# Performance work log

Measured on AMD Instinct MI355X. Metric: run time of the kernel, lower is better.

The kernel has to match this reference:

```python
import jax, jax.numpy as jnp
import numpy as np

B, S, E, H, D, P = 4, 2048, 1024, 16, 64, 64  # batch, seq, embed, heads, head_dim, position_dim
MASKED_BIAS = -10000.0


def setup_inputs() -> dict:
    key = jax.random.key(0)
    ks = jax.random.split(key, 24)
    n = lambda k, sh: jax.random.normal(k, sh, dtype=jnp.float32)
    eyeD = jnp.eye(D, dtype=jnp.float32)
    eyeH = jnp.eye(H, dtype=jnp.float32)
    inp = {
        'hidden_states': n(ks[0], (B, S, E)),
        'position_states': n(ks[1], (B, S, P)),
        # Conv2D per-head projections (identity init + perturbation): [H, D, D]
        'Wq': eyeD[None] + 0.02 * n(ks[2], (H, D, D)), 'bq': 0.01 * n(ks[3], (H, D)),
        'Wk': eyeD[None] + 0.02 * n(ks[4], (H, D, D)), 'bk': 0.01 * n(ks[5], (H, D)),
        'Wv': eyeD[None] + 0.02 * n(ks[6], (H, D, D)), 'bv': 0.01 * n(ks[7], (H, D)),
        # Conv2D(transpose=True) cross-head mix: weight [H_out, H_in, D], bias [H, D]
        'Wqh': eyeH[:, :, None] + 0.02 * n(ks[8], (H, H, D)), 'bqh': 0.01 * n(ks[9], (H, D)),
        'Wkh': eyeH[:, :, None] + 0.02 * n(ks[10], (H, H, D)), 'bkh': 0.01 * n(ks[11], (H, D)),
        'Wvh': eyeH[:, :, None] + 0.02 * n(ks[12], (H, H, D)), 'bvh': 0.01 * n(ks[13], (H, D)),
        # p_attn Conv1D: position_dim -> 3*head_dim
        'Wp': 0.02 * n(ks[14], (P, 3 * D)), 'bp': 0.01 * n(ks[15], (3 * D,)),
        # position_conv expand: weight [3, 1, H], bias [H]
        'Wpe': 0.02 * n(ks[16], (3, 1, H)), 'bpe': 0.01 * n(ks[17], (H,)),
        # c_proj Conv1D: E -> E
        'Wc': 0.02 * n(ks[18], (E, E)), 'bc': 0.01 * n(ks[19], (E,)),
    }
    return inp


def _attention(hidden_states, position_states, Wq, bq, Wqh, bqh, Wk, bk, Wkh, bkh,
               Wv, bv, Wvh, bvh, Wp, bp, Wpe, bpe, Wc, bc):
    b, s, _ = hidden_states.shape
    x = hidden_states.reshape(b, s, H, D)

    def proj(Wa, ba, Wh, bh):
        # Conv2D: per-head linear within head_dim
        y = jnp.einsum('bshd,hde->bshe', x, Wa) + ba
        # Conv2D(transpose): mix across heads, per feature dim d
        return jnp.einsum('bshd,ghd->bsgd', y, Wh) + bh

    q = proj(Wq, bq, Wqh, bqh)  # [b,s,H,D]
    k = proj(Wk, bk, Wkh, bkh)
    v = proj(Wv, bv, Wvh, bvh)

    # p_attn (Conv1D) -> [b,s,3,D]; p_expand broadcasts each var across heads
    p = (position_states @ Wp + bp).reshape(b, s, 3, D)
    pe = p[..., None, :] * Wpe[:, 0, :][:, :, None] + bpe[:, None]  # [b,s,3,H,D]
    q = q + pe[:, :, 0]
    k = k + pe[:, :, 1]
    v = v + pe[:, :, 2]

    q = q.transpose(0, 2, 1, 3)  # [b,H,s,D]
    k = k.transpose(0, 2, 1, 3)
    v = v.transpose(0, 2, 1, 3)

    scores = jnp.einsum('bhqd,bhkd->bhqk', q, k) / jnp.sqrt(jnp.float32(D))
    causal = jnp.tril(jnp.ones((s, s), dtype=bool))
    scores = jnp.where(causal, scores, jnp.float32(MASKED_BIAS))
    w = jax.nn.softmax(scores, axis=-1)
    o = jnp.einsum('bhqk,bhkd->bhqd', w, v)
    o = o.transpose(0, 2, 1, 3).reshape(b, s, E)
    return o @ Wc + bc


def reference(hidden_states, position_states, Wq, bq, Wqh, bqh, Wk, bk, Wkh, bkh,
              Wv, bv, Wvh, bvh, Wp, bp, Wpe, bpe, Wc, bc):
    return _attention(hidden_states, position_states, Wq, bq, Wqh, bqh, Wk, bk,
                      Wkh, bkh, Wv, bv, Wvh, bvh, Wp, bp, Wpe, bpe, Wc, bc)
```

## Files before the change

kernel.cpp:

```cpp
#include <hip/hip_runtime.h>
#include <stdint.h>
#include <stddef.h>

using bf16x8 = __attribute__((ext_vector_type(8))) __bf16;
using f32x4  = __attribute__((ext_vector_type(4))) float;
using u16x8  = __attribute__((ext_vector_type(8))) unsigned short;
using u16x4  = __attribute__((ext_vector_type(4))) unsigned short;
typedef unsigned short u16;

#define DEV __device__ __forceinline__

#define QSCALE 0.18033688011112042f
#define SBIAS 32.0f

DEV u16 f2bf(float f) {
  unsigned u = __float_as_uint(f);
  u += 0x7fffu + ((u >> 16) & 1u);
  return (u16)(u >> 16);
}

DEV void gld_lds16(const u16* g, u16* l) {
  __builtin_amdgcn_global_load_lds(
      (__attribute__((address_space(1))) void*)g,
      (__attribute__((address_space(3))) void*)l, 16, 0, 0);
}

__global__ __launch_bounds__(256) void k_prep(const float* __restrict__ hs, const float* __restrict__ ps,
                                              const float* __restrict__ Wq, const float* __restrict__ Wk,
                                              const float* __restrict__ Wv, const float* __restrict__ Wqh,
                                              const float* __restrict__ Wkh, const float* __restrict__ Wvh,
                                              const float* __restrict__ Wp, const float* __restrict__ Wpe,
                                              const float* __restrict__ bq, const float* __restrict__ bk,
                                              const float* __restrict__ bv, const float* __restrict__ bqh,
                                              const float* __restrict__ bkh, const float* __restrict__ bvh,
                                              const float* __restrict__ bp, const float* __restrict__ bpe,
                                              const float* __restrict__ Wc,
                                              u16* __restrict__ A, u16* __restrict__ Wt,
                                              float* __restrict__ bias, u16* __restrict__ WcT) {
  const int bid = blockIdx.x;
  if (bid < 8704) {
    int idx = bid * 256 + threadIdx.x;
    int t  = idx / 272;
    int c4 = (idx - t * 272) * 4;
    float4 f;
    if (c4 < 1024) f = *(const float4*)(hs + (size_t)t * 1024 + c4);
    else           f = *(const float4*)(ps + (size_t)t * 64 + (c4 - 1024));
    u16x4 o4;
    o4[0] = f2bf(f.x); o4[1] = f2bf(f.y); o4[2] = f2bf(f.z); o4[3] = f2bf(f.w);
    *(u16x4*)(A + (size_t)t * 1088 + c4) = o4;
  } else if (bid < 21760) {
    int idx = (bid - 8704) * 256 + threadIdx.x;
    int n = idx / 1088, kk = idx - n * 1088;
    int which = n >> 10, g = (n >> 6) & 15, e = n & 63;
    const float* Wa = (which == 0) ? Wq : (which == 1) ? Wk : Wv;
    const float* Wh = (which == 0) ? Wqh : (which == 1) ? Wkh : Wvh;
    float val;
    if (kk < 1024) {
      int h = kk >> 6, d = kk & 63;
      val = Wa[(size_t)(h * 64 + d) * 64 + e] * Wh[(size_t)(g * 16 + h) * 64 + e];
    } else {
      int p = kk - 1024;
      val = Wp[(size_t)p * 192 + which * 64 + e] * Wpe[which * 16 + g];
    }
    if (which == 0) val *= QSCALE;
    Wt[idx] = f2bf(val);
  } else if (bid < 21772) {
    int n = (bid - 21760) * 256 + threadIdx.x;
    int which = n >> 10, g = (n >> 6) & 15, e = n & 63;
    const float* ba = (which == 0) ? bq : (which == 1) ? bk : bv;
    const float* Wh = (which == 0) ? Wqh : (which == 1) ? Wkh : Wvh;
    const float* bh = (which == 0) ? bqh : (which == 1) ? bkh : bvh;
    float s = bh[g * 64 + e] + bp[which * 64 + e] * Wpe[which * 16 + g] + bpe[g];
    for (int h = 0; h < 16; ++h) s += ba[h * 64 + e] * Wh[(g * 16 + h) * 64 + e];
    if (which == 0) s *= QSCALE;
    bias[n] = s;
  } else {
    __shared__ float tile[32][33];
    int t = bid - 21772;
    int tx = threadIdx.x & 31, ty = threadIdx.x >> 5;
    int n0 = (t & 31) * 32, k0 = (t >> 5) * 32;
#pragma unroll
    for (int i = 0; i < 32; i += 8)
      tile[ty + i][tx] = Wc[(size_t)(k0 + ty + i) * 1024 + n0 + tx];
    __syncthreads();
#pragma unroll
    for (int i = 0; i < 32; i += 8)
      WcT[(size_t)(n0 + ty + i) * 1024 + k0 + tx] = f2bf(tile[tx][ty + i]);
  }
}

template <int EPI>
__global__ __launch_bounds__(256) void gemm128(const u16* __restrict__ A, const u16* __restrict__ Bt,
                                               const float* __restrict__ bias,
                                               u16* __restrict__ qo, u16* __restrict__ ko, u16* __restrict__ vo,
                                               float* __restrict__ outf, int M, int N, int K, int NT) {
  __shared__ alignas(16) u16 As[2][8192];
  __shared__ alignas(16) u16 Bs[2][8192];
  const int tid = threadIdx.x;
  const int l = tid & 63, w = tid >> 6;
  const int lr = l & 15, lg = l >> 4;
  const int wm = w >> 1, wn = w & 1;

  const int nwg = gridDim.x;
  const int cpx = nwg >> 3;
  const int virt = (blockIdx.x & 7) * cpx + (blockIdx.x >> 3);
  const int m0 = (virt / NT) * 128, n0 = (virt - (virt / NT) * NT) * 128;

  const int KT = K >> 6;

  f32x4 acc[4][4] = {};

#pragma unroll
  for (int call = 0; call < 4; ++call) {
    int ci = (call * 4 + w) * 64 + l;
    int row = ci >> 3, s = ci & 7;
    int kq = (s ^ (row & 7)) * 8;
    gld_lds16(A + (size_t)(m0 + row) * K + kq, &As[0][(call * 4 + w) * 512]);
    gld_lds16(Bt + (size_t)(n0 + row) * K + kq, &Bs[0][(call * 4 + w) * 512]);
  }

  int cur = 0;
  for (int kt = 0; kt < KT; ++kt) {
    if (kt + 1 < KT) {
      const int kb = (kt + 1) * 64;
#pragma unroll
      for (int call = 0; call < 4; ++call) {
        int ci = (call * 4 + w) * 64 + l;
        int row = ci >> 3, s = ci & 7;
        int kq = (s ^ (row & 7)) * 8;
        gld_lds16(A + (size_t)(m0 + row) * K + kb + kq, &As[cur ^ 1][(call * 4 + w) * 512]);
        gld_lds16(Bt + (size_t)(n0 + row) * K + kb + kq, &Bs[cur ^ 1][(call * 4 + w) * 512]);
      }
      asm volatile("s_waitcnt vmcnt(8)" ::: "memory");
    } else {
      asm volatile("s_waitcnt vmcnt(0)" ::: "memory");
    }
    __builtin_amdgcn_s_barrier();
    asm volatile("" ::: "memory");

    const u16* AsC = As[cur];
    const u16* BsC = Bs[cur];
#pragma unroll
    for (int kk = 0; kk < 2; ++kk) {
      bf16x8 af[4], bfr[4];
#pragma unroll
      for (int mf = 0; mf < 4; ++mf) {
        int row = wm * 64 + mf * 16 + lr;
        int byo = row * 128 + (((kk * 32 + lg * 8) * 2) ^ ((row & 7) << 4));
        af[mf] = *(const bf16x8*)((const char*)AsC + byo);
      }
#pragma unroll
      for (int nf = 0; nf < 4; ++nf) {
        int row = wn * 64 + nf * 16 + lr;
        int byo = row * 128 + (((kk * 32 + lg * 8) * 2) ^ ((row & 7) << 4));
        bfr[nf] = *(const bf16x8*)((const char*)BsC + byo);
      }
      __builtin_amdgcn_s_setprio(1);
#pragma unroll
      for (int mf = 0; mf < 4; ++mf)
#pragma unroll
        for (int nf = 0; nf < 4; ++nf)
          acc[mf][nf] = __builtin_amdgcn_mfma_f32_16x16x32_bf16(af[mf], bfr[nf], acc[mf][nf], 0, 0, 0);
      __builtin_amdgcn_s_setprio(0);
    }

    asm volatile("s_waitcnt lgkmcnt(0)" ::: "memory");
    __builtin_amdgcn_s_barrier();
    asm volatile("" ::: "memory");
    cur ^= 1;
  }

#pragma unroll
  for (int mf = 0; mf < 4; ++mf)
#pragma unroll
    for (int nf = 0; nf < 4; ++nf)
#pragma unroll
      for (int r = 0; r < 4; ++r) {
        int row = m0 + wm * 64 + mf * 16 + lg * 4 + r;
        int col = n0 + wn * 64 + nf * 16 + lr;
        float val = acc[mf][nf][r] + bias[col];
        if (EPI == 0) {
          int which = col >> 10, g = (col >> 6) & 15, e = col & 63;
          int b = row >> 11, si = row & 2047;
          size_t idx = ((size_t)((b * 16 + g) * 2048 + si)) * 64 + e;
          u16 bvv = f2bf(val);
          if (which == 0) qo[idx] = bvv;
          else if (which == 1) ko[idx] = bvv;
          else vo[idx] = bvv;
        } else {
          outf[(size_t)row * N + col] = val;
        }
      }
}

__global__ __launch_bounds__(256) void k_transV(const u16* __restrict__ v, u16* __restrict__ vT) {
  __shared__ u16 t[64][65];
  int bh = blockIdx.y, s0 = blockIdx.x * 64;
  const u16* src = v + ((size_t)bh * 2048 + s0) * 64;
  u16* dst = vT + (size_t)bh * 64 * 2048 + s0;
  int tid = threadIdx.x;
#pragma unroll
  for (int it = 0; it < 2; ++it) {
    int ci = it * 256 + tid;
    int row = ci >> 3, sl = ci & 7;
    u16x8 val = *(const u16x8*)(src + (size_t)row * 64 + sl * 8);
#pragma unroll
    for (int jj = 0; jj < 8; ++jj) t[row][sl * 8 + jj] = val[jj];
  }
  __syncthreads();
#pragma unroll
  for (int it = 0; it < 2; ++it) {
    int ci = it * 256 + tid;
    int d = ci >> 3, sl = ci & 7;
    u16x8 val;
#pragma unroll
    for (int jj = 0; jj < 8; ++jj) {
      int cp = sl * 8 + jj;
      int tt = (cp & 3) * 16 + (cp >> 2);
      val[jj] = t[tt][d];
    }
    *(u16x8*)(dst + (size_t)d * 2048 + sl * 8) = val;
  }
}

__global__ __launch_bounds__(512) void k_attn(const u16* __restrict__ q, const u16* __restrict__ k,
                                              const u16* __restrict__ vt, u16* __restrict__ o) {
  __shared__ alignas(16) u16 Ks[2][4096];
  __shared__ alignas(16) u16 Vs[2][4096];
  __shared__ alignas(16) u16 Ps[8][32 * 72];

  const int tid = threadIdx.x, l = tid & 63, w = tid >> 6;
  const int lr = l & 15, lg = l >> 4;
  const int i = blockIdx.x;
  const int bh = (i & 7) * 8 + ((i >> 3) & 7);
  const int tile = 7 - (i >> 6);
  const int b = bh >> 4, h = bh & 15;

  const u16* qp = q + (size_t)bh * 2048 * 64;
  const u16* kp = k + (size_t)bh * 2048 * 64;
  const u16* vp = vt + (size_t)bh * 64 * 2048;

  const int srow = tid >> 3;
  const int skq = ((tid & 7) ^ (srow & 7)) * 8;

  bf16x8 ones;
#pragma unroll
  for (int e = 0; e < 8; ++e) ones[e] = (__bf16)1.0f;

  const int qr0 = tile * 256 + w * 32;
  const int jmax = 4 * tile + 3;
  const int jmask = qr0 >> 6;

  bf16x8 qf[2][2];
#pragma unroll
  for (int mf = 0; mf < 2; ++mf)
#pragma unroll
    for (int kk = 0; kk < 2; ++kk)
      qf[mf][kk] = *(const bf16x8*)(qp + (size_t)(qr0 + mf * 16 + lr) * 64 + kk * 32 + lg * 8);

  f32x4 oacc[2][4] = {};
  f32x4 osum[2] = {};

  gld_lds16(kp + (size_t)srow * 64 + skq, &Ks[0][w * 512]);
  gld_lds16(vp + (size_t)srow * 2048 + skq, &Vs[0][w * 512]);

  int cur = 0;
  for (int j = 0; j <= jmax; ++j) {
    if (j < jmax) {
      const int jn = j + 1;
      gld_lds16(kp + (size_t)(jn * 64 + srow) * 64 + skq, &Ks[cur ^ 1][w * 512]);
      gld_lds16(vp + (size_t)srow * 2048 + jn * 64 + skq, &Vs[cur ^ 1][w * 512]);
      asm volatile("s_waitcnt vmcnt(2)" ::: "memory");
    } else {
      asm volatile("s_waitcnt vmcnt(0)" ::: "memory");
    }
    __builtin_amdgcn_s_barrier();
    asm volatile("" ::: "memory");

    if (j <= jmask) {
      const u16* KsC = Ks[cur];
      const u16* VsC = Vs[cur];

      f32x4 sfr[2][4];
#pragma unroll
      for (int mf = 0; mf < 2; ++mf)
#pragma unroll
        for (int nf = 0; nf < 4; ++nf)
          sfr[mf][nf] = f32x4{-SBIAS, -SBIAS, -SBIAS, -SBIAS};
#pragma unroll
      for (int kk = 0; kk < 2; ++kk) {
        bf16x8 bk[4];
#pragma unroll
        for (int nf = 0; nf < 4; ++nf) {
          int row = nf * 16 + lr;
          int byo = row * 128 + (((kk * 32 + lg * 8) * 2) ^ ((row & 7) << 4));
          bk[nf] = *(const bf16x8*)((const char*)KsC + byo);
        }
        __builtin_amdgcn_s_setprio(1);
#pragma unroll
        for (int mf = 0; mf < 2; ++mf)
#pragma unroll
          for (int nf = 0; nf < 4; ++nf)
            sfr[mf][nf] = __builtin_amdgcn_mfma_f32_16x16x32_bf16(qf[mf][kk], bk[nf], sfr[mf][nf], 0, 0, 0);
        __builtin_amdgcn_s_setprio(0);
      }

      const bool maskt = (j == jmask);
#pragma unroll
      for (int mf = 0; mf < 2; ++mf)
#pragma unroll
        for (int r = 0; r < 4; ++r) {
          float s0 = sfr[mf][0][r], s1 = sfr[mf][1][r], s2 = sfr[mf][2][r], s3 = sfr[mf][3][r];
          if (maskt) {
            int rowg = qr0 + mf * 16 + lg * 4 + r;
            int base = j * 64 + lr;
            if (base      > rowg) s0 = -1e30f;
            if (base + 16 > rowg) s1 = -1e30f;
            if (base + 32 > rowg) s2 = -1e30f;
            if (base + 48 > rowg) s3 = -1e30f;
          }
          float p0 = __builtin_amdgcn_exp2f(s0);
          float p1 = __builtin_amdgcn_exp2f(s1);
          float p2 = __builtin_amdgcn_exp2f(s2);
          float p3 = __builtin_amdgcn_exp2f(s3);
          unsigned w0, w1;
          asm("v_cvt_pk_bf16_f32 %0, %1, %2" : "=v"(w0) : "v"(p0), "v"(p1));
          asm("v_cvt_pk_bf16_f32 %0, %1, %2" : "=v"(w1) : "v"(p2), "v"(p3));
          uint2 pw; pw.x = w0; pw.y = w1;
          *(uint2*)&Ps[w][(mf * 16 + lg * 4 + r) * 72 + 4 * lr] = pw;
        }

#pragma unroll
      for (int kk = 0; kk < 2; ++kk) {
        bf16x8 pa[2];
#pragma unroll
        for (int mf = 0; mf < 2; ++mf)
          pa[mf] = *(const bf16x8*)&Ps[w][(mf * 16 + lr) * 72 + kk * 32 + lg * 8];
        bf16x8 bv[4];
#pragma unroll
        for (int df = 0; df < 4; ++df) {
          int row = df * 16 + lr;
          int byo = row * 128 + (((kk * 32 + lg * 8) * 2) ^ ((row & 7) << 4));
          bv[df] = *(const bf16x8*)((const char*)VsC + byo);
        }
        __builtin_amdgcn_s_setprio(1);
#pragma unroll
        for (int mf = 0; mf < 2; ++mf)
#pragma unroll
          for (int df = 0; df < 4; ++df)
            oacc[mf][df] = __builtin_amdgcn_mfma_f32_16x16x32_bf16(pa[mf], bv[df], oacc[mf][df], 0, 0, 0);
#pragma unroll
        for (int mf = 0; mf < 2; ++mf)
          osum[mf] = __builtin_amdgcn_mfma_f32_16x16x32_bf16(pa[mf], ones, osum[mf], 0, 0, 0);
        __builtin_amdgcn_s_setprio(0);
      }
    }

    asm volatile("s_waitcnt lgkmcnt(0)" ::: "memory");
    __builtin_amdgcn_s_barrier();
    asm volatile("" ::: "memory");
    cur ^= 1;
  }

#pragma unroll
  for (int mf = 0; mf < 2; ++mf)
#pragma unroll
    for (int r = 0; r < 4; ++r) {
      float inv = 1.0f / osum[mf][r];
      int rowg = qr0 + mf * 16 + lg * 4 + r;
#pragma unroll
      for (int df = 0; df < 4; ++df)
        o[((size_t)(b * 2048 + rowg)) * 1024 + h * 64 + df * 16 + lr] = f2bf(oacc[mf][df][r] * inv);
    }
}

extern "C" void kernel_launch(void* const* d_in, const int* in_sizes, int n_in,
                              void* d_out, int out_size, void* d_ws, size_t ws_size,
                              hipStream_t stream) {
  const float* hs  = (const float*)d_in[0];
  const float* pos = (const float*)d_in[1];
  const float* Wq  = (const float*)d_in[2];  const float* bq  = (const float*)d_in[3];
  const float* Wk  = (const float*)d_in[4];  const float* bk  = (const float*)d_in[5];
  const float* Wv  = (const float*)d_in[6];  const float* bv  = (const float*)d_in[7];
  const float* Wqh = (const float*)d_in[8];  const float* bqh = (const float*)d_in[9];
  const float* Wkh = (const float*)d_in[10]; const float* bkh = (const float*)d_in[11];
  const float* Wvh = (const float*)d_in[12]; const float* bvh = (const float*)d_in[13];
  const float* Wp  = (const float*)d_in[14]; const float* bp  = (const float*)d_in[15];
  const float* Wpe = (const float*)d_in[16]; const float* bpe = (const float*)d_in[17];
  const float* Wc  = (const float*)d_in[18]; const float* bc  = (const float*)d_in[19];
  float* out = (float*)d_out;
  char* ws = (char*)d_ws;

  u16*   Abf   = (u16*)  (ws + 0);
  u16*   WT    = (u16*)  (ws + 17825792);
  float* biasq = (float*)(ws + 24510464);
  u16*   WcT   = (u16*)  (ws + 24522752);
  u16*   qb_   = (u16*)  (ws + 26619904);
  u16*   kb_   = (u16*)  (ws + 43397120);
  u16*   vb_   = (u16*)  (ws + 60174336);
  u16*   vTb   = (u16*)  (ws + 76951552);
  u16*   ob    = Abf;

  k_prep<<<22796, 256, 0, stream>>>(hs, pos, Wq, Wk, Wv, Wqh, Wkh, Wvh, Wp, Wpe,
                                    bq, bk, bv, bqh, bkh, bvh, bp, bpe, Wc,
                                    Abf, WT, biasq, WcT);
  gemm128<0><<<1536, 256, 0, stream>>>(Abf, WT, biasq, qb_, kb_, vb_, nullptr, 8192, 3072, 1088, 24);
  k_transV<<<dim3(32, 64), 256, 0, stream>>>(vb_, vTb);
  k_attn<<<512, 512, 0, stream>>>(qb_, kb_, vTb, ob);
  gemm128<1><<<512, 256, 0, stream>>>(ob, WcT, bc, nullptr, nullptr, nullptr, out, 8192, 1024, 1024, 8);
}
```

Measured before the change: 185.2 us.

## Replace QKV GEMM with 256x192-tile 512-thread kernel and split-phase staging

Adds a dedicated QKV projection GEMM that uses 256x192 output tiles with 8 waves and 512 blocks, replacing the 128x128 tile, 1536-block launch. Staging of the next K tile is split into B and two A halves, interleaved with four compute phases under barriers and vmcnt waits. The larger tiles raise arithmetic intensity and reduce redundant global reads, and 512 blocks map to a single wave of workgroups across the CUs. In exchange it uses about 112KB of LDS and more accumulator registers, which lowers occupancy. The generic gemm128 is reduced to the output-projection epilogue only.

```diff
diff --git a/kernel.cpp b/kernel.cpp
--- a/kernel.cpp
+++ b/kernel.cpp
@@ -89,10 +89,122 @@
   }
 }
 
-template <int EPI>
+__global__ __launch_bounds__(512) void gemmQKV(const u16* __restrict__ A, const u16* __restrict__ Bt,
+                                               const float* __restrict__ bias,
+                                               u16* __restrict__ qo, u16* __restrict__ ko, u16* __restrict__ vo,
+                                               int K) {
+  __shared__ alignas(16) u16 As[2][16384];
+  __shared__ alignas(16) u16 Bs[2][12288];
+  const int tid = threadIdx.x;
+  const int l = tid & 63, w = tid >> 6;
+  const int lr = l & 15, lg = l >> 4;
+  const int wm = w >> 2, wn = w & 3;
+
+  const int virt = (blockIdx.x & 7) * 64 + (blockIdx.x >> 3);
+  const int m0 = (virt >> 4) * 256, n0 = (virt & 15) * 192;
+
+#define STAGE_B(buf, kt) do {                                                  \
+  _Pragma("unroll")                                                            \
+  for (int c = 0; c < 3; ++c) {                                                \
+    int ci = c * 512 + tid;                                                    \
+    int srow = ci >> 3, s = ci & 7;                                            \
+    int kq = (s ^ (srow & 7)) * 8;                                             \
+    gld_lds16(Bt + (size_t)(n0 + srow) * K + (kt) * 64 + kq,                   \
+              &Bs[buf][(c * 8 + w) * 512]);                                    \
+  } } while (0)
+
+#define STAGE_A(buf, h, kt) do {                                               \
+  _Pragma("unroll")                                                            \
+  for (int c = 0; c < 2; ++c) {                                                \
+    int ci = c * 512 + tid;                                                    \
+    int srow = ci >> 3, s = ci & 7;                                            \
+    int g = (h) * 64 + (srow & 63) + (srow >> 6) * 128;                        \
+    int kq = (s ^ (srow & 7)) * 8;                                             \
+    gld_lds16(A + (size_t)(m0 + g) * K + (kt) * 64 + kq,                       \
+              &As[buf][(h) * 8192 + (c * 8 + w) * 512]);                       \
+  } } while (0)
+
+  f32x4 acc[8][3] = {};
+
+#define PHASE(buf, mh, kk) do {                                                \
+  bf16x8 af[4], bfr[3];                                                        \
+  _Pragma("unroll")                                                            \
+  for (int mq = 0; mq < 4; ++mq) {                                             \
+    int lrow = (mh) * 128 + wm * 64 + mq * 16 + lr;                            \
+    int byo = lrow * 128 + ((((kk) * 32 + lg * 8) * 2) ^ ((lrow & 7) << 4));   \
+    af[mq] = *(const bf16x8*)((const char*)As[buf] + byo);                     \
+  }                                                                            \
+  _Pragma("unroll")                                                            \
+  for (int nf = 0; nf < 3; ++nf) {                                             \
+    int brow = wn * 48 + nf * 16 + lr;                                         \
+    int byo = brow * 128 + ((((kk) * 32 + lg * 8) * 2) ^ ((brow & 7) << 4));   \
+    bfr[nf] = *(const bf16x8*)((const char*)Bs[buf] + byo);                    \
+  }                                                                            \
+  __builtin_amdgcn_s_setprio(1);                                               \
+  _Pragma("unroll")                                                            \
+  for (int mq = 0; mq < 4; ++mq)                                               \
+    _Pragma("unroll")                                                          \
+    for (int nf = 0; nf < 3; ++nf)                                             \
+      acc[(mh) * 4 + mq][nf] = __builtin_amdgcn_mfma_f32_16x16x32_bf16(        \
+          af[mq], bfr[nf], acc[(mh) * 4 + mq][nf], 0, 0, 0);                   \
+  __builtin_amdgcn_s_setprio(0);                                               \
+} while (0)
+
+  STAGE_B(0, 0);
+  STAGE_A(0, 0, 0);
+  STAGE_A(0, 1, 0);
+
+  const int KT = 17;
+  for (int t = 0; t < KT; ++t) {
+    const int buf = t & 1;
+    asm volatile("s_waitcnt vmcnt(2)" ::: "memory");
+    __builtin_amdgcn_s_barrier();
+    asm volatile("" ::: "memory");
+    if (t + 1 < KT) STAGE_B(buf ^ 1, t + 1);
+    PHASE(buf, 0, 0);
+    __builtin_amdgcn_s_barrier();
+    asm volatile("" ::: "memory");
+    if (t + 1 < KT) STAGE_A(buf ^ 1, 0, t + 1);
+    PHASE(buf, 0, 1);
+    if (t + 1 < KT) {
+      asm volatile("s_waitcnt vmcnt(5)" ::: "memory");
+    } else {
+      asm volatile("s_waitcnt vmcnt(0)" ::: "memory");
+    }
+    __builtin_amdgcn_s_barrier();
+    asm volatile("" ::: "memory");
+    if (t + 1 < KT) STAGE_A(buf ^ 1, 1, t + 1);
+    PHASE(buf, 1, 0);
+    __builtin_amdgcn_s_barrier();
+    asm volatile("" ::: "memory");
+    PHASE(buf, 1, 1);
+  }
+
+#undef PHASE
+#undef STAGE_A
+#undef STAGE_B
+
+#pragma unroll
+  for (int mf = 0; mf < 8; ++mf)
+#pragma unroll
+    for (int nf = 0; nf < 3; ++nf)
+#pragma unroll
+      for (int r = 0; r < 4; ++r) {
+        int row = m0 + wm * 128 + (mf >> 2) * 64 + (mf & 3) * 16 + lg * 4 + r;
+        int col = n0 + wn * 48 + nf * 16 + lr;
+        float val = acc[mf][nf][r] + bias[col];
+        int which = col >> 10, g = (col >> 6) & 15, e = col & 63;
+        int b = row >> 11, si = row & 2047;
+        size_t idx = ((size_t)((b * 16 + g) * 2048 + si)) * 64 + e;
+        u16 bvv = f2bf(val);
+        if (which == 0) qo[idx] = bvv;
+        else if (which == 1) ko[idx] = bvv;
+        else vo[idx] = bvv;
+      }
+}
+
 __global__ __launch_bounds__(256) void gemm128(const u16* __restrict__ A, const u16* __restrict__ Bt,
                                                const float* __restrict__ bias,
-                                               u16* __restrict__ qo, u16* __restrict__ ko, u16* __restrict__ vo,
                                                float* __restrict__ outf, int M, int N, int K, int NT) {
   __shared__ alignas(16) u16 As[2][8192];
   __shared__ alignas(16) u16 Bs[2][8192];
@@ -178,18 +290,7 @@
       for (int r = 0; r < 4; ++r) {
         int row = m0 + wm * 64 + mf * 16 + lg * 4 + r;
         int col = n0 + wn * 64 + nf * 16 + lr;
-        float val = acc[mf][nf][r] + bias[col];
-        if (EPI == 0) {
-          int which = col >> 10, g = (col >> 6) & 15, e = col & 63;
-          int b = row >> 11, si = row & 2047;
-          size_t idx = ((size_t)((b * 16 + g) * 2048 + si)) * 64 + e;
-          u16 bvv = f2bf(val);
-          if (which == 0) qo[idx] = bvv;
-          else if (which == 1) ko[idx] = bvv;
-          else vo[idx] = bvv;
-        } else {
-          outf[(size_t)row * N + col] = val;
-        }
+        outf[(size_t)row * N + col] = acc[mf][nf][r] + bias[col];
       }
 }
 
@@ -404,8 +505,8 @@
   k_prep<<<22796, 256, 0, stream>>>(hs, pos, Wq, Wk, Wv, Wqh, Wkh, Wvh, Wp, Wpe,
                                     bq, bk, bv, bqh, bkh, bvh, bp, bpe, Wc,
                                     Abf, WT, biasq, WcT);
-  gemm128<0><<<1536, 256, 0, stream>>>(Abf, WT, biasq, qb_, kb_, vb_, nullptr, 8192, 3072, 1088, 24);
+  gemmQKV<<<512, 512, 0, stream>>>(Abf, WT, biasq, qb_, kb_, vb_, 1088);
   k_transV<<<dim3(32, 64), 256, 0, stream>>>(vb_, vTb);
   k_attn<<<512, 512, 0, stream>>>(qb_, kb_, vTb, ob);
-  gemm128<1><<<512, 256, 0, stream>>>(ob, WcT, bc, nullptr, nullptr, nullptr, out, 8192, 1024, 1024, 8);
-}
+  gemm128<<<512, 256, 0, stream>>>(ob, WcT, bc, out, 8192, 1024, 1024, 8);
+}
```

Result: slower. 198.0 us (+6.9%).

## Keep softmax probabilities in registers by computing transposed scores

Applied to the files above, without the earlier changes.

The QK^T MFMA now takes its operands swapped, so each lane holds score elements laid out as the A-operand fragment for the PV MFMA. The probabilities are packed straight into bf16x8 registers, which removes the per-wave LDS staging buffer Ps and its write/read round trip. To make this layout match, the V-transpose kernel permutes the key order within each 64-key block. Launch bounds now request 4 waves per SIMD, which may cap registers per thread and cause spills.

```diff
diff --git a/kernel.cpp b/kernel.cpp
--- a/kernel.cpp
+++ b/kernel.cpp
@@ -216,18 +216,18 @@
 #pragma unroll
     for (int jj = 0; jj < 8; ++jj) {
       int cp = sl * 8 + jj;
-      int tt = (cp & 3) * 16 + (cp >> 2);
+      int kk = cp >> 5, lgp = (cp >> 3) & 3, ii = cp & 7;
+      int tt = kk * 32 + (ii >> 2) * 16 + lgp * 4 + (ii & 3);
       val[jj] = t[tt][d];
     }
     *(u16x8*)(dst + (size_t)d * 2048 + sl * 8) = val;
   }
 }
 
-__global__ __launch_bounds__(512) void k_attn(const u16* __restrict__ q, const u16* __restrict__ k,
-                                              const u16* __restrict__ vt, u16* __restrict__ o) {
+__global__ __launch_bounds__(512, 4) void k_attn(const u16* __restrict__ q, const u16* __restrict__ k,
+                                                 const u16* __restrict__ vt, u16* __restrict__ o) {
   __shared__ alignas(16) u16 Ks[2][4096];
   __shared__ alignas(16) u16 Vs[2][4096];
-  __shared__ alignas(16) u16 Ps[8][32 * 72];
 
   const int tid = threadIdx.x, l = tid & 63, w = tid >> 6;
   const int lr = l & 15, lg = l >> 4;
@@ -301,41 +301,40 @@
         for (int mf = 0; mf < 2; ++mf)
 #pragma unroll
           for (int nf = 0; nf < 4; ++nf)
-            sfr[mf][nf] = __builtin_amdgcn_mfma_f32_16x16x32_bf16(qf[mf][kk], bk[nf], sfr[mf][nf], 0, 0, 0);
+            sfr[mf][nf] = __builtin_amdgcn_mfma_f32_16x16x32_bf16(bk[nf], qf[mf][kk], sfr[mf][nf], 0, 0, 0);
         __builtin_amdgcn_s_setprio(0);
       }
 
       const bool maskt = (j == jmask);
-#pragma unroll
-      for (int mf = 0; mf < 2; ++mf)
-#pragma unroll
-        for (int r = 0; r < 4; ++r) {
-          float s0 = sfr[mf][0][r], s1 = sfr[mf][1][r], s2 = sfr[mf][2][r], s3 = sfr[mf][3][r];
-          if (maskt) {
-            int rowg = qr0 + mf * 16 + lg * 4 + r;
-            int base = j * 64 + lr;
-            if (base      > rowg) s0 = -1e30f;
-            if (base + 16 > rowg) s1 = -1e30f;
-            if (base + 32 > rowg) s2 = -1e30f;
-            if (base + 48 > rowg) s3 = -1e30f;
+      bf16x8 pa[2][2];
+#pragma unroll
+      for (int mf = 0; mf < 2; ++mf) {
+        const int qg = qr0 + mf * 16 + lr;
+        float p[4][4];
+#pragma unroll
+        for (int nf = 0; nf < 4; ++nf) {
+          int base = j * 64 + nf * 16 + lg * 4;
+#pragma unroll
+          for (int r = 0; r < 4; ++r) {
+            float s = sfr[mf][nf][r];
+            if (maskt && (base + r > qg)) s = -1e30f;
+            p[nf][r] = __builtin_amdgcn_exp2f(s);
           }
-          float p0 = __builtin_amdgcn_exp2f(s0);
-          float p1 = __builtin_amdgcn_exp2f(s1);
-          float p2 = __builtin_amdgcn_exp2f(s2);
-          float p3 = __builtin_amdgcn_exp2f(s3);
-          unsigned w0, w1;
-          asm("v_cvt_pk_bf16_f32 %0, %1, %2" : "=v"(w0) : "v"(p0), "v"(p1));
-          asm("v_cvt_pk_bf16_f32 %0, %1, %2" : "=v"(w1) : "v"(p2), "v"(p3));
-          uint2 pw; pw.x = w0; pw.y = w1;
-          *(uint2*)&Ps[w][(mf * 16 + lg * 4 + r) * 72 + 4 * lr] = pw;
         }
+#pragma unroll
+        for (int kk = 0; kk < 2; ++kk) {
+          unsigned a0, a1, a2, a3;
+          asm("v_cvt_pk_bf16_f32 %0, %1, %2" : "=v"(a0) : "v"(p[2 * kk][0]),     "v"(p[2 * kk][1]));
+          asm("v_cvt_pk_bf16_f32 %0, %1, %2" : "=v"(a1) : "v"(p[2 * kk][2]),     "v"(p[2 * kk][3]));
+          asm("v_cvt_pk_bf16_f32 %0, %1, %2" : "=v"(a2) : "v"(p[2 * kk + 1][0]), "v"(p[2 * kk + 1][1]));
+          asm("v_cvt_pk_bf16_f32 %0, %1, %2" : "=v"(a3) : "v"(p[2 * kk + 1][2]), "v"(p[2 * kk + 1][3]));
+          uint4 uu; uu.x = a0; uu.y = a1; uu.z = a2; uu.w = a3;
+          pa[mf][kk] = *(bf16x8*)&uu;
+        }
+      }
 
 #pragma unroll
       for (int kk = 0; kk < 2; ++kk) {
-        bf16x8 pa[2];
-#pragma unroll
-        for (int mf = 0; mf < 2; ++mf)
-          pa[mf] = *(const bf16x8*)&Ps[w][(mf * 16 + lr) * 72 + kk * 32 + lg * 8];
         bf16x8 bv[4];
 #pragma unroll
         for (int df = 0; df < 4; ++df) {
@@ -348,10 +347,10 @@
         for (int mf = 0; mf < 2; ++mf)
 #pragma unroll
           for (int df = 0; df < 4; ++df)
-            oacc[mf][df] = __builtin_amdgcn_mfma_f32_16x16x32_bf16(pa[mf], bv[df], oacc[mf][df], 0, 0, 0);
+            oacc[mf][df] = __builtin_amdgcn_mfma_f32_16x16x32_bf16(pa[mf][kk], bv[df], oacc[mf][df], 0, 0, 0);
 #pragma unroll
         for (int mf = 0; mf < 2; ++mf)
-          osum[mf] = __builtin_amdgcn_mfma_f32_16x16x32_bf16(pa[mf], ones, osum[mf], 0, 0, 0);
+          osum[mf] = __builtin_amdgcn_mfma_f32_16x16x32_bf16(pa[mf][kk], ones, osum[mf], 0, 0, 0);
         __builtin_amdgcn_s_setprio(0);
       }
     }
```

Result: faster. 178.3 us, median of 2 (-3.7%).
